# Kernel tuning notes

Hardware: AMD Instinct MI355X
Metric: run time of the kernel (lower is better)

## Reference

```python
import jax, jax.numpy as jnp
import numpy as np

EPS = 1e-17       # utils.EPS in tkipf/compile
NEG_INF = -1e30   # utils.NEG_INF
B, T, V, H, L, S = 256, 128, 512, 256, 64, 4
TEMP_B = 1.0


def setup_inputs() -> dict:
    key = jax.random.key(0)
    ks = jax.random.split(key, 12)

    def lin(k, o, i):  # torch nn.Linear default init: U(-1/sqrt(in), 1/sqrt(in))
        s = 1.0 / np.sqrt(i)
        kw, kb = jax.random.split(k)
        return (jax.random.uniform(kw, (o, i), jnp.float32, -s, s),
                jax.random.uniform(kb, (o,), jnp.float32, -s, s))

    w_ih, b_ih = lin(ks[0], 4 * H, H)   # LSTMCell input weights (i,f,g,o)
    w_hh, b_hh = lin(ks[1], 4 * H, H)
    wz1, bz1 = lin(ks[2], H, H)         # head_z_1
    wz2, bz2 = lin(ks[3], 2 * L, H)     # head_z_2 (gaussian: mu, log_var)
    wb1, bb1 = lin(ks[4], H, H)         # head_b_1
    wb2, bb2 = lin(ks[5], 1, H)         # head_b_2
    wd1, bd1 = lin(ks[6], H, L)         # decode_1
    wd2, bd2 = lin(ks[7], V, H)         # decode_2
    embed_w = jax.random.normal(ks[8], (V, H), jnp.float32)  # nn.Embedding N(0,1)
    inputs = jax.random.randint(ks[9], (B, T), 0, V)
    lengths = jax.random.randint(ks[10], (B,), 1, T + 1)
    return dict(embed_w=embed_w, w_ih=w_ih, w_hh=w_hh, b_ih=b_ih, b_hh=b_hh,
                wz1=wz1, bz1=bz1, wz2=wz2, bz2=bz2, wb1=wb1, bb1=bb1,
                wb2=wb2, bb2=bb2, wd1=wd1, bd1=bd1, wd2=wd2, bd2=bd2,
                inputs=inputs, lengths=lengths)


def _forward(embed_w, w_ih, w_hh, b_ih, b_hh, wz1, bz1, wz2, bz2,
             wb1, bb1, wb2, bb2, wd1, bd1, wd2, bd2, inputs, lengths):
    nkey = jax.random.key(42)  # fixed sampling noise (training path, evaluate=False)
    emb = embed_w[inputs]      # [B,T,H]

    def lstm_step(carry, xm):
        h, c = carry
        x, m = xm              # x: [B,H], m: [B] mask for this step
        gates = x @ w_ih.T + b_ih + h @ w_hh.T + b_hh
        i, f, g, o = jnp.split(gates, 4, axis=1)
        c2 = jax.nn.sigmoid(f) * c + jax.nn.sigmoid(i) * jnp.tanh(g)
        h2 = jax.nn.sigmoid(o) * jnp.tanh(c2)
        h2 = m[:, None] * h2
        c2 = m[:, None] * c2
        return (h2, c2), h2

    def masked_encode(mask):
        init = (jnp.zeros((B, H), emb.dtype), jnp.zeros((B, H), emb.dtype))
        _, hs = jax.lax.scan(lstm_step, init, (emb.transpose(1, 0, 2), mask.T))
        return hs.transpose(1, 0, 2)  # [B,T,H]

    mask = jnp.ones((B, T), jnp.float32)
    log_cum_acc = jnp.zeros((B, T), jnp.float32)  # sum of log-cumsums over segments
    encs, recs, masks = [], [], []
    b_logits, b_samples, z_logits, z_samples = [], [], [], []

    for seg in range(S):  # small fixed structural loop (max_num_segments)
        enc = masked_encode(mask)
        encs.append(enc)

        # --- boundaries b ---
        if seg == S - 1:
            sample_b = jax.nn.one_hot(lengths - 1, T, dtype=jnp.float32)
        else:
            hid = jax.nn.relu(enc @ wb1.T + bb1)
            lb = (hid @ wb2.T + bb2)[..., 0]  # [B,T]
            lb = jnp.concatenate([jnp.full((B, 1), NEG_INF, jnp.float32), lb[:, 1:]], axis=1)
            u = jax.random.uniform(jax.random.fold_in(nkey, 2 * seg), (B, T), jnp.float32)
            gumbel = -jnp.log(EPS - jnp.log(u + EPS))
            sample_b = jax.nn.softmax((lb + gumbel) / TEMP_B, axis=-1)
            b_logits.append(lb)
        b_samples.append(sample_b)

        # --- latents z (gaussian) ---
        readout = jnp.sum(enc[:, :-1] * sample_b[:, 1:, None], axis=1)  # [B,H]
        lz = jax.nn.relu(readout @ wz1.T + bz1) @ wz2.T + bz2           # [B,2L]
        mu, log_var = jnp.split(lz, 2, axis=1)
        eps_z = jax.random.normal(jax.random.fold_in(nkey, 2 * seg + 1), (B, L), jnp.float32)
        sample_z = mu + jnp.exp(0.5 * log_var) * eps_z
        z_logits.append(lz)
        z_samples.append(sample_z)

        # --- next-segment hidden-state mask: prod of cumsums (in log space) ---
        log_cum_acc = log_cum_acc + jnp.log(jnp.cumsum(sample_b, axis=1) + EPS)
        if seg < S - 1:
            mask = jnp.exp(log_cum_acc)
            masks.append(mask)

        # --- decode: single step repeated over full sequence ---
        pred = jax.nn.relu(sample_z @ wd1.T + bd1) @ wd2.T + bd2        # [B,V]
        recs.append(jnp.broadcast_to(pred[:, None, :], (B, T, V)))

    return (jnp.stack(encs), jnp.stack(recs), jnp.stack(masks),
            jnp.stack(b_logits), jnp.stack(b_samples),
            jnp.stack(z_logits), jnp.stack(z_samples))


def reference(embed_w, w_ih, w_hh, b_ih, b_hh, wz1, bz1, wz2, bz2,
              wb1, bb1, wb2, bb2, wd1, bd1, wd2, bd2, inputs, lengths):
    return _forward(embed_w, w_ih, w_hh, b_ih, b_hh, wz1, bz1, wz2, bz2,
                    wb1, bb1, wb2, bb2, wd1, bd1, wd2, bd2, inputs, lengths)
```

## Files before the change

kernel.cpp:

```cpp
#include <hip/hip_runtime.h>
#include <hip/hip_bf16.h>

#define RNG_VARIANT 2

typedef __attribute__((ext_vector_type(8))) short bf16x8;
typedef __attribute__((ext_vector_type(4))) float f32x4;

__host__ __device__ inline void tf2x32(unsigned k0, unsigned k1,
                                       unsigned x0, unsigned x1,
                                       unsigned* r0, unsigned* r1) {
  unsigned ks2 = k0 ^ k1 ^ 0x1BD11BDAu;
#define TFR(r) { x0 += x1; x1 = (x1 << r) | (x1 >> (32 - r)); x1 ^= x0; }
  x0 += k0; x1 += k1;
  TFR(13) TFR(15) TFR(26) TFR(6)  x0 += k1;  x1 += ks2 + 1u;
  TFR(17) TFR(29) TFR(16) TFR(24) x0 += ks2; x1 += k0 + 2u;
  TFR(13) TFR(15) TFR(26) TFR(6)  x0 += k0;  x1 += k1 + 3u;
  TFR(17) TFR(29) TFR(16) TFR(24) x0 += k1;  x1 += ks2 + 4u;
  TFR(13) TFR(15) TFR(26) TFR(6)  x0 += ks2; x1 += k0 + 5u;
#undef TFR
  *r0 = x0; *r1 = x1;
}

__device__ __forceinline__ unsigned rng_bits32(unsigned k0, unsigned k1,
                                               unsigned n, unsigned half) {
#if RNG_VARIANT == 2
  unsigned o0, o1; tf2x32(k0, k1, 0u, n, &o0, &o1); return o0 ^ o1;
#elif RNG_VARIANT == 1
  unsigned o0, o1; tf2x32(k0, k1, 0u, n, &o0, &o1); return o1;
#else
  unsigned i0 = (n < half) ? n : n - half;
  unsigned o0, o1; tf2x32(k0, k1, i0, i0 + half, &o0, &o1);
  return (n < half) ? o0 : o1;
#endif
}

__device__ __forceinline__ float bits_to_unit(unsigned bits) {
  return __uint_as_float((bits >> 9) | 0x3f800000u) - 1.0f;
}

__device__ __forceinline__ unsigned short f2bf(float x) {
  union { float f; unsigned u; } v; v.f = x;
  unsigned r = v.u + 0x7fffu + ((v.u >> 16) & 1u);
  return (unsigned short)(r >> 16);
}
__device__ __forceinline__ float bf2f(unsigned short h) {
  return __uint_as_float(((unsigned)h) << 16);
}

__device__ __forceinline__ float sigm(float x) {
  return 1.0f / (1.0f + __expf(-x));
}
__device__ __forceinline__ float tanh_f(float x) {
  float ax = fabsf(x);
  float e = __expf(-2.0f * ax);
  float t = (1.0f - e) / (1.0f + e);
  return copysignf(t, x);
}

__device__ __forceinline__ float erfinv_f(float x) {
  float w = -log1pf(-x * x);
  float p;
  if (w < 5.0f) {
    w -= 2.5f;
    p = 2.81022636e-08f;
    p = fmaf(p, w, 3.43273939e-07f);
    p = fmaf(p, w, -3.5233877e-06f);
    p = fmaf(p, w, -4.39150654e-06f);
    p = fmaf(p, w, 0.00021858087f);
    p = fmaf(p, w, -0.00125372503f);
    p = fmaf(p, w, -0.00417768164f);
    p = fmaf(p, w, 0.246640727f);
    p = fmaf(p, w, 1.50140941f);
  } else {
    w = sqrtf(w) - 3.0f;
    p = -0.000200214257f;
    p = fmaf(p, w, 0.000100950558f);
    p = fmaf(p, w, 0.00134934322f);
    p = fmaf(p, w, -0.00367342844f);
    p = fmaf(p, w, 0.00573950773f);
    p = fmaf(p, w, -0.0076224613f);
    p = fmaf(p, w, 0.00943887047f);
    p = fmaf(p, w, 1.00167406f);
    p = fmaf(p, w, 2.83297682f);
  }
  return p * x;
}

__global__ void prep_k(const float* __restrict__ w_ih, const float* __restrict__ w_hh,
                       const float* __restrict__ wb1, const float* __restrict__ b_ih,
                       const float* __restrict__ b_hh,
                       unsigned short* __restrict__ wih_b, unsigned short* __restrict__ wpk,
                       unsigned short* __restrict__ wb1_b, float* __restrict__ biasg,
                       unsigned int* __restrict__ flags) {
  int i = blockIdx.x * 256 + threadIdx.x;
  for (int idx = i; idx < 262144; idx += 65536) wih_b[idx] = f2bf(w_ih[idx]);
  if (i < 65536) wb1_b[i] = f2bf(wb1[i]);
  if (i < 1024) biasg[i] = b_ih[i] + b_hh[i];
  if (i >= 1024 && i < 2048) flags[i - 1024] = 0u;
  if (i < 32768) {
    int l = i & 63, ks = (i >> 6) & 7, tile = i >> 9;
    int n = tile * 16 + (l & 15);
    int kb = ks * 32 + (l >> 4) * 8;
    const float* src = w_hh + (size_t)n * 256 + kb;
#pragma unroll
    for (int j = 0; j < 8; ++j) wpk[(size_t)i * 8 + j] = f2bf(src[j]);
  }
}

__global__ void embed_k(const int* __restrict__ inputs, const float* __restrict__ embw,
                        unsigned short* __restrict__ emb) {
  int bt = blockIdx.x, h = threadIdx.x;
  emb[(size_t)bt * 256 + h] = f2bf(embw[(size_t)inputs[bt] * 256 + h]);
}

__global__ __launch_bounds__(256) void gemm_bf16(
    const unsigned short* __restrict__ A, const unsigned short* __restrict__ Bt,
    const float* __restrict__ bias, float* __restrict__ outF,
    unsigned short* __restrict__ outB, int M, int N, int K, int relu) {
  __shared__ __align__(16) unsigned short As[128][40];
  __shared__ __align__(16) unsigned short Bs[128][40];
  int tid = threadIdx.x;
  int m0 = blockIdx.x * 128, n0 = blockIdx.y * 128;
  int w = tid >> 6, l = tid & 63;
  int wr = w >> 1, wc = w & 1;
  int lr = l & 15, lq = l >> 4;
  f32x4 acc[4][4];
#pragma unroll
  for (int i = 0; i < 4; ++i)
#pragma unroll
    for (int j = 0; j < 4; ++j) acc[i][j] = (f32x4)(0.0f);
  int sr = tid >> 2, sk = (tid & 3) * 8;
#pragma unroll 1
  for (int kc = 0; kc < K; kc += 32) {
#pragma unroll
    for (int p = 0; p < 2; ++p) {
      int row = sr + p * 64;
      *(bf16x8*)&As[row][sk] = *(const bf16x8*)(A + (size_t)(m0 + row) * K + kc + sk);
      *(bf16x8*)&Bs[row][sk] = *(const bf16x8*)(Bt + (size_t)(n0 + row) * K + kc + sk);
    }
    __syncthreads();
    bf16x8 af[4], bfr[4];
#pragma unroll
    for (int i = 0; i < 4; ++i) {
      af[i] = *(const bf16x8*)&As[wr * 64 + i * 16 + lr][lq * 8];
      bfr[i] = *(const bf16x8*)&Bs[wc * 64 + i * 16 + lr][lq * 8];
    }
#pragma unroll
    for (int i = 0; i < 4; ++i)
#pragma unroll
      for (int j = 0; j < 4; ++j)
        acc[i][j] = __builtin_amdgcn_mfma_f32_16x16x32_bf16(af[i], bfr[j], acc[i][j], 0, 0, 0);
    __syncthreads();
  }
#pragma unroll
  for (int i = 0; i < 4; ++i)
#pragma unroll
    for (int j = 0; j < 4; ++j) {
      int col = n0 + wc * 64 + j * 16 + lr;
      float bv = bias ? bias[col] : 0.0f;
#pragma unroll
      for (int q = 0; q < 4; ++q) {
        int row = m0 + wr * 64 + i * 16 + lq * 4 + q;
        float v = acc[i][j][q] + bv;
        if (relu) v = fmaxf(v, 0.0f);
        size_t o = (size_t)row * N + col;
        if (outF) outF[o] = v;
        if (outB) outB[o] = f2bf(v);
      }
    }
}

template <bool XWF32>
__global__ __launch_bounds__(256, 1) void lstm_lds(
    const unsigned short* __restrict__ Wpk, const void* __restrict__ xw_,
    const float* __restrict__ mask_buf, int use_mask,
    float* __restrict__ enc_out, unsigned short* __restrict__ enc_b,
    unsigned int* flags, unsigned int flag_base) {
  __shared__ __align__(16) unsigned short Wl[65536];
  const int tid = threadIdx.x;
  const int w = tid >> 6, l = tid & 63;
  const int lr = l & 15, lq = l >> 4;
  const int rg = blockIdx.x >> 2, cb = blockIdx.x & 3;
  const int batch = rg * 16 + lr;
  const int nsub = cb * 64 + w * 16 + lq * 4;

  {
    const int4* src4 = (const int4*)Wpk;
    int4* dst4 = (int4*)Wl;
#pragma unroll
    for (int it = 0; it < 32; ++it) {
      int d = tid + it * 256;
      int tile = d >> 9, within = d & 511;
      int g = tile >> 2, wv = tile & 3;
      dst4[d] = src4[(size_t)(g * 16 + cb * 4 + wv) * 512 + within];
    }
  }
  __syncthreads();

  float cst[4] = {0.f, 0.f, 0.f, 0.f};
  unsigned int* flag = flags + rg * 64;

  const float* xwf = (const float*)xw_;
  const unsigned short* xwb = (const unsigned short*)xw_;
  f32x4 xwf4[4];
  uint2 xwu2[4];
  float mvp;

#define PREFETCH(T)                                                          \
  {                                                                          \
    size_t base_ = ((size_t)batch * 128 + (T)) * 1024 + nsub;                \
    _Pragma("unroll") for (int g = 0; g < 4; ++g) {                          \
      if (XWF32)                                                             \
        xwf4[g] = *(const f32x4*)(xwf + base_ + g * 256);                    \
      else                                                                   \
        xwu2[g] = *(const uint2*)(xwb + base_ + g * 256);                    \
    }                                                                        \
    mvp = use_mask ? mask_buf[batch * 128 + (T)] : 1.0f;                     \
  }

  PREFETCH(0);

#pragma unroll 1
  for (int t = 0; t < 128; ++t) {
    f32x4 acc[4];
#pragma unroll
    for (int g = 0; g < 4; ++g) {
      if (XWF32) {
        acc[g] = xwf4[g];
      } else {
        acc[g][0] = __uint_as_float(xwu2[g].x << 16);
        acc[g][1] = __uint_as_float(xwu2[g].x & 0xffff0000u);
        acc[g][2] = __uint_as_float(xwu2[g].y << 16);
        acc[g][3] = __uint_as_float(xwu2[g].y & 0xffff0000u);
      }
    }
    float mv = mvp;

    if (t < 127) PREFETCH(t + 1);

    int woff = 0;
    asm volatile("" : "+v"(woff));
    bf16x8 Wf[4][8];
#pragma unroll
    for (int g = 0; g < 4; ++g)
#pragma unroll
      for (int ks = 0; ks < 8; ++ks)
        Wf[g][ks] = *(const bf16x8*)(Wl + woff + ((g * 4 + w) << 12) +
                                     (ks << 9) + (l << 3));
#pragma unroll
    for (int g = 0; g < 4; ++g)
#pragma unroll
      for (int ks = 0; ks < 8; ++ks)
        asm volatile("" : "+v"(Wf[g][ks]));

    if (t > 0) {
      unsigned thr = flag_base + 4u * (unsigned)t;
      while (__hip_atomic_load(flag, __ATOMIC_RELAXED, __HIP_MEMORY_SCOPE_AGENT) < thr)
        __builtin_amdgcn_s_sleep(1);
      const unsigned short* hrow = enc_b + ((size_t)batch * 128 + (t - 1)) * 256;
      bf16x8 af[8];
#pragma unroll
      for (int ks = 0; ks < 8; ++ks)
        af[ks] = *(const bf16x8*)(hrow + ks * 32 + lq * 8);
#pragma unroll
      for (int ks = 0; ks < 8; ++ks)
#pragma unroll
        for (int g = 0; g < 4; ++g)
          acc[g] = __builtin_amdgcn_mfma_f32_16x16x32_bf16(Wf[g][ks], af[ks],
                                                           acc[g], 0, 0, 0);
    }

    float hv[4];
#pragma unroll
    for (int q = 0; q < 4; ++q) {
      float ig = acc[0][q], fg = acc[1][q], gg = acc[2][q], og = acc[3][q];
      float cn = sigm(fg) * cst[q] + sigm(ig) * tanh_f(gg);
      float hq = sigm(og) * tanh_f(cn);
      hq *= mv;
      cn *= mv;
      cst[q] = cn;
      hv[q] = hq;
    }
    size_t eo = ((size_t)batch * 128 + t) * 256 + nsub;
    f32x4 hvv;
    hvv[0] = hv[0]; hvv[1] = hv[1]; hvv[2] = hv[2]; hvv[3] = hv[3];
    *(f32x4*)(enc_out + eo) = hvv;
    unsigned long long pk =
        (unsigned long long)f2bf(hv[0]) |
        ((unsigned long long)f2bf(hv[1]) << 16) |
        ((unsigned long long)f2bf(hv[2]) << 32) |
        ((unsigned long long)f2bf(hv[3]) << 48);
    __hip_atomic_store((unsigned long long*)(enc_b + eo), pk,
                       __ATOMIC_RELAXED, __HIP_MEMORY_SCOPE_AGENT);

    asm volatile("s_waitcnt vmcnt(0)" ::: "memory");
    __syncthreads();
    if (tid == 0)
      __hip_atomic_fetch_add(flag, 1u, __ATOMIC_RELAXED, __HIP_MEMORY_SCOPE_AGENT);
  }
#undef PREFETCH
}

__global__ __launch_bounds__(512) void gemv_lb(const unsigned short* __restrict__ hid,
                                               const float* __restrict__ wb2,
                                               const float* __restrict__ bb2,
                                               float* __restrict__ lb) {
  int l = threadIdx.x & 63, w = threadIdx.x >> 6;
  int row = blockIdx.x * 8 + w;
  const unsigned short* hp = hid + (size_t)row * 256 + l * 4;
  uint2 hv = *(const uint2*)hp;
  float4 wv = *(const float4*)(wb2 + l * 4);
  float s = bf2f((unsigned short)(hv.x & 0xffff)) * wv.x +
            bf2f((unsigned short)(hv.x >> 16)) * wv.y +
            bf2f((unsigned short)(hv.y & 0xffff)) * wv.z +
            bf2f((unsigned short)(hv.y >> 16)) * wv.w;
#pragma unroll
  for (int d = 32; d > 0; d >>= 1) s += __shfl_xor(s, d);
  if (l == 0) lb[row] = s + bb2[0];
}

__global__ __launch_bounds__(128) void boundary_k(
    const float* __restrict__ lb, int seg, unsigned k0, unsigned k1,
    float* __restrict__ blog, float* __restrict__ bsamp, float* __restrict__ masks_o,
    float* __restrict__ lca, float* __restrict__ maskb) {
  int b = blockIdx.x, t = threadIdx.x;
  int l = t & 63, w = t >> 6;
  float v = lb[b * 128 + t];
  if (t == 0) v = -1e30f;
  unsigned bits = rng_bits32(k0, k1, (unsigned)(b * 128 + t), 16384u);
  float u = bits_to_unit(bits);
  float g = -logf(1e-17f - logf(u + 1e-17f));
  float y = v + g;
  float m = y;
#pragma unroll
  for (int d = 32; d > 0; d >>= 1) m = fmaxf(m, __shfl_xor(m, d));
  __shared__ float xs[2];
  if (l == 0) xs[w] = m;
  __syncthreads();
  m = fmaxf(xs[0], xs[1]);
  float e = expf(y - m);
  float ssum = e;
#pragma unroll
  for (int d = 32; d > 0; d >>= 1) ssum += __shfl_xor(ssum, d);
  __shared__ float ss2[2];
  if (l == 0) ss2[w] = ssum;
  __syncthreads();
  ssum = ss2[0] + ss2[1];
  float sb = e / ssum;
  blog[b * 128 + t] = v;
  bsamp[b * 128 + t] = sb;
  float cs = sb;
#pragma unroll
  for (int d = 1; d < 64; d <<= 1) {
    float p = __shfl_up(cs, d);
    if (l >= d) cs += p;
  }
  __shared__ float wt[2];
  if (l == 63) wt[w] = cs;
  __syncthreads();
  if (w == 1) cs += wt[0];
  float lg = logf(cs + 1e-17f);
  float a = (seg == 0 ? 0.0f : lca[b * 128 + t]) + lg;
  lca[b * 128 + t] = a;
  float mk = expf(a);
  maskb[b * 128 + t] = mk;
  masks_o[b * 128 + t] = mk;
}

__global__ __launch_bounds__(128) void onehot_k(const int* __restrict__ lengths,
                                                float* __restrict__ bsamp) {
  int b = blockIdx.x, t = threadIdx.x;
  bsamp[b * 128 + t] = (t == lengths[b] - 1) ? 1.0f : 0.0f;
}

__global__ __launch_bounds__(256) void readout_k(const float* __restrict__ enc,
                                                 const float* __restrict__ sb,
                                                 float* __restrict__ rout) {
  int b = blockIdx.x, h = threadIdx.x;
  __shared__ float sl[128];
  if (h < 128) sl[h] = sb[b * 128 + h];
  __syncthreads();
  float a = 0.0f;
  const float* ep = enc + (size_t)b * 128 * 256 + h;
#pragma unroll 4
  for (int t2 = 0; t2 < 127; ++t2) a += ep[(size_t)t2 * 256] * sl[t2 + 1];
  rout[b * 256 + h] = a;
}

__global__ __launch_bounds__(128) void zhead_k(
    const float* __restrict__ rout, const float* __restrict__ wz1,
    const float* __restrict__ bz1, const float* __restrict__ wz2,
    const float* __restrict__ bz2, unsigned k0, unsigned k1,
    float* __restrict__ zlo, float* __restrict__ zsa, float* __restrict__ zbuf) {
  int b = blockIdx.x, t = threadIdx.x;
  __shared__ float rl[256], hz[256], lzs[128];
  rl[t] = rout[b * 256 + t];
  rl[t + 128] = rout[b * 256 + t + 128];
  __syncthreads();
  for (int h = t; h < 256; h += 128) {
    float a = bz1[h];
    const float* wp = wz1 + (size_t)h * 256;
    for (int k2 = 0; k2 < 256; ++k2) a += rl[k2] * wp[k2];
    hz[h] = fmaxf(a, 0.0f);
  }
  __syncthreads();
  {
    float a = bz2[t];
    const float* wp = wz2 + (size_t)t * 256;
    for (int k2 = 0; k2 < 256; ++k2) a += hz[k2] * wp[k2];
    zlo[b * 128 + t] = a;
    lzs[t] = a;
  }
  __syncthreads();
  if (t < 64) {
    unsigned bits = rng_bits32(k0, k1, (unsigned)(b * 64 + t), 8192u);
    float f = bits_to_unit(bits);
    const float LO = -0x1.fffffep-1f;
    float u = fmaxf(LO, f * 2.0f + LO);
    float ez = 1.4142135623730951f * erfinv_f(u);
    float z = lzs[t] + expf(0.5f * lzs[t + 64]) * ez;
    zsa[b * 64 + t] = z;
    zbuf[b * 64 + t] = z;
  }
}

__global__ __launch_bounds__(256) void decode_k(
    const float* __restrict__ zbuf, const float* __restrict__ wd1,
    const float* __restrict__ bd1, const float* __restrict__ wd2,
    const float* __restrict__ bd2, float* __restrict__ pred) {
  int b = blockIdx.x, t = threadIdx.x;
  __shared__ float zl[64], hd[256];
  if (t < 64) zl[t] = zbuf[b * 64 + t];
  __syncthreads();
  {
    float a = bd1[t];
    const float* wp = wd1 + (size_t)t * 64;
    for (int k2 = 0; k2 < 64; ++k2) a += zl[k2] * wp[k2];
    hd[t] = fmaxf(a, 0.0f);
  }
  __syncthreads();
  for (int v2 = t; v2 < 512; v2 += 256) {
    float p = bd2[v2];
    const float* wp = wd2 + (size_t)v2 * 256;
    for (int k2 = 0; k2 < 256; ++k2) p += hd[k2] * wp[k2];
    pred[b * 512 + v2] = p;
  }
}

__global__ __launch_bounds__(128) void bcast_k(const float* __restrict__ pred,
                                               float* __restrict__ recs) {
  int bt = blockIdx.x;
  int b = bt >> 7;
  float4 v = ((const float4*)(pred + (size_t)b * 512))[threadIdx.x];
  ((float4*)(recs + (size_t)bt * 512))[threadIdx.x] = v;
}

extern "C" void kernel_launch(void* const* d_in, const int* in_sizes, int n_in,
                              void* d_out, int out_size, void* d_ws, size_t ws_size,
                              hipStream_t stream) {
  const float* embed_w = (const float*)d_in[0];
  const float* w_ih = (const float*)d_in[1];
  const float* w_hh = (const float*)d_in[2];
  const float* b_ih = (const float*)d_in[3];
  const float* b_hh = (const float*)d_in[4];
  const float* wz1 = (const float*)d_in[5];
  const float* bz1 = (const float*)d_in[6];
  const float* wz2 = (const float*)d_in[7];
  const float* bz2 = (const float*)d_in[8];
  const float* wb1 = (const float*)d_in[9];
  const float* bb1 = (const float*)d_in[10];
  const float* wb2 = (const float*)d_in[11];
  const float* bb2 = (const float*)d_in[12];
  const float* wd1 = (const float*)d_in[13];
  const float* bd1 = (const float*)d_in[14];
  const float* wd2 = (const float*)d_in[15];
  const float* bd2 = (const float*)d_in[16];
  const int* inputs = (const int*)d_in[17];
  const int* lengths = (const int*)d_in[18];

  char* ws = (char*)d_ws;
  size_t off = 0;
  auto alloc = [&](size_t n) { char* p = ws + off; off += (n + 255) & ~(size_t)255; return p; };
  unsigned short* wih_b = (unsigned short*)alloc((size_t)1024 * 256 * 2);
  unsigned short* wpk   = (unsigned short*)alloc((size_t)1024 * 256 * 2);
  unsigned short* wb1_b = (unsigned short*)alloc((size_t)256 * 256 * 2);
  float* biasg = (float*)alloc(1024 * 4);
  unsigned int* flags = (unsigned int*)alloc(1024 * 4);
  unsigned short* bufA  = (unsigned short*)alloc((size_t)32768 * 256 * 2);
  unsigned short* enc_b = (unsigned short*)alloc((size_t)32768 * 256 * 2);
  float* lb    = (float*)alloc((size_t)32768 * 4);
  float* lca   = (float*)alloc((size_t)32768 * 4);
  float* maskb = (float*)alloc((size_t)32768 * 4);
  float* rout  = (float*)alloc((size_t)256 * 256 * 4);
  float* zbuf  = (float*)alloc((size_t)256 * 64 * 4);
  float* pred  = (float*)alloc((size_t)256 * 512 * 4);
  size_t fixed = off;
  bool xwf32 = (ws_size >= fixed + (size_t)32768 * 1024 * 4);
  void* xw = alloc(xwf32 ? (size_t)32768 * 1024 * 4 : (size_t)32768 * 1024 * 2);

  unsigned kb[4][2], kz[4][2];
  for (int s = 0; s < 4; ++s) {
    tf2x32(0u, 42u, 0u, (unsigned)(2 * s), &kb[s][0], &kb[s][1]);
    tf2x32(0u, 42u, 0u, (unsigned)(2 * s + 1), &kz[s][0], &kz[s][1]);
  }

  float* out = (float*)d_out;
  float* encs = out;
  float* recs = out + 33554432;
  float* masks = out + 100663296;
  float* blog = out + 100761600;
  float* bsamp = out + 100859904;
  float* zlog = out + 100990976;
  float* zsamp = out + 101122048;

  prep_k<<<256, 256, 0, stream>>>(w_ih, w_hh, wb1, b_ih, b_hh, wih_b, wpk, wb1_b,
                                  biasg, flags);
  embed_k<<<32768, 256, 0, stream>>>(inputs, embed_w, bufA);
  {
    dim3 g(32768 / 128, 1024 / 128);
    gemm_bf16<<<g, 256, 0, stream>>>(bufA, wih_b, biasg,
                                     xwf32 ? (float*)xw : nullptr,
                                     xwf32 ? nullptr : (unsigned short*)xw,
                                     32768, 1024, 256, 0);
  }

  for (int seg = 0; seg < 4; ++seg) {
    unsigned fb = (unsigned)seg * 512u;
    if (xwf32)
      lstm_lds<true><<<64, 256, 0, stream>>>(wpk, xw, maskb, seg > 0 ? 1 : 0,
                                             encs + (size_t)seg * 8388608, enc_b,
                                             flags, fb);
    else
      lstm_lds<false><<<64, 256, 0, stream>>>(wpk, xw, maskb, seg > 0 ? 1 : 0,
                                              encs + (size_t)seg * 8388608, enc_b,
                                              flags, fb);

    if (seg < 3) {
      dim3 g(32768 / 128, 256 / 128);
      gemm_bf16<<<g, 256, 0, stream>>>(enc_b, wb1_b, bb1, nullptr, bufA,
                                       32768, 256, 256, 1);
      gemv_lb<<<4096, 512, 0, stream>>>(bufA, wb2, bb2, lb);
      boundary_k<<<256, 128, 0, stream>>>(lb, seg, kb[seg][0], kb[seg][1],
                                          blog + (size_t)seg * 32768,
                                          bsamp + (size_t)seg * 32768,
                                          masks + (size_t)seg * 32768, lca, maskb);
    } else {
      onehot_k<<<256, 128, 0, stream>>>(lengths, bsamp + (size_t)3 * 32768);
    }
    readout_k<<<256, 256, 0, stream>>>(encs + (size_t)seg * 8388608,
                                       bsamp + (size_t)seg * 32768, rout);
    zhead_k<<<256, 128, 0, stream>>>(rout, wz1, bz1, wz2, bz2, kz[seg][0], kz[seg][1],
                                     zlog + (size_t)seg * 32768,
                                     zsamp + (size_t)seg * 16384, zbuf);
    decode_k<<<256, 256, 0, stream>>>(zbuf, wd1, bd1, wd2, bd2, pred);
    bcast_k<<<32768, 128, 0, stream>>>(pred, recs + (size_t)seg * 16777216);
  }
}
```

Measured before the change: 2.105 ms.

## Replace per-step counter flags with sentinel-value polling on LSTM hidden state

The per-step atomic counter handshake between the blocks of a row group is removed. Each consumer now polls the previous step's hidden-state values directly, treating a 0xffff bf16 pattern as 'not yet written'. Before every segment a fill kernel resets enc_b to that sentinel, and the block-to-(row,col) mapping is changed. This drops the waitcnt, block barrier and atomic increment from each of the 128 serial steps, at the cost of an extra 16MB fill per segment and a correctness risk if a real hidden value ever encodes as 0xffff.

```diff
diff --git a/kernel.cpp b/kernel.cpp
--- a/kernel.cpp
+++ b/kernel.cpp
@@ -90,13 +90,11 @@
                        const float* __restrict__ wb1, const float* __restrict__ b_ih,
                        const float* __restrict__ b_hh,
                        unsigned short* __restrict__ wih_b, unsigned short* __restrict__ wpk,
-                       unsigned short* __restrict__ wb1_b, float* __restrict__ biasg,
-                       unsigned int* __restrict__ flags) {
+                       unsigned short* __restrict__ wb1_b, float* __restrict__ biasg) {
   int i = blockIdx.x * 256 + threadIdx.x;
   for (int idx = i; idx < 262144; idx += 65536) wih_b[idx] = f2bf(w_ih[idx]);
   if (i < 65536) wb1_b[i] = f2bf(wb1[i]);
   if (i < 1024) biasg[i] = b_ih[i] + b_hh[i];
-  if (i >= 1024 && i < 2048) flags[i - 1024] = 0u;
   if (i < 32768) {
     int l = i & 63, ks = (i >> 6) & 7, tile = i >> 9;
     int n = tile * 16 + (l & 15);
@@ -111,6 +109,11 @@
                         unsigned short* __restrict__ emb) {
   int bt = blockIdx.x, h = threadIdx.x;
   emb[(size_t)bt * 256 + h] = f2bf(embw[(size_t)inputs[bt] * 256 + h]);
+}
+
+__global__ void fill_sent(uint4* __restrict__ p) {
+  uint4 v; v.x = v.y = v.z = v.w = 0xffffffffu;
+  p[blockIdx.x * 256 + threadIdx.x] = v;
 }
 
 __global__ __launch_bounds__(256) void gemm_bf16(
@@ -171,16 +174,15 @@
 }
 
 template <bool XWF32>
-__global__ __launch_bounds__(256, 1) void lstm_lds(
+__global__ __launch_bounds__(256, 1) void lstm_poll(
     const unsigned short* __restrict__ Wpk, const void* __restrict__ xw_,
     const float* __restrict__ mask_buf, int use_mask,
-    float* __restrict__ enc_out, unsigned short* __restrict__ enc_b,
-    unsigned int* flags, unsigned int flag_base) {
+    float* __restrict__ enc_out, unsigned short* __restrict__ enc_b) {
   __shared__ __align__(16) unsigned short Wl[65536];
   const int tid = threadIdx.x;
   const int w = tid >> 6, l = tid & 63;
   const int lr = l & 15, lq = l >> 4;
-  const int rg = blockIdx.x >> 2, cb = blockIdx.x & 3;
+  const int rg = blockIdx.x & 15, cb = blockIdx.x >> 4;
   const int batch = rg * 16 + lr;
   const int nsub = cb * 64 + w * 16 + lq * 4;
 
@@ -198,7 +200,6 @@
   __syncthreads();
 
   float cst[4] = {0.f, 0.f, 0.f, 0.f};
-  unsigned int* flag = flags + rg * 64;
 
   const float* xwf = (const float*)xw_;
   const unsigned short* xwb = (const unsigned short*)xw_;
@@ -254,14 +255,31 @@
         asm volatile("" : "+v"(Wf[g][ks]));
 
     if (t > 0) {
-      unsigned thr = flag_base + 4u * (unsigned)t;
-      while (__hip_atomic_load(flag, __ATOMIC_RELAXED, __HIP_MEMORY_SCOPE_AGENT) < thr)
-        __builtin_amdgcn_s_sleep(1);
-      const unsigned short* hrow = enc_b + ((size_t)batch * 128 + (t - 1)) * 256;
+      const unsigned long long* hq =
+          (const unsigned long long*)(enc_b + ((size_t)batch * 128 + (t - 1)) * 256);
+      unsigned long long rv[16];
+      while (true) {
+#pragma unroll
+        for (int i = 0; i < 8; ++i) {
+          rv[2 * i] = __hip_atomic_load(hq + i * 8 + lq * 2,
+                                        __ATOMIC_RELAXED, __HIP_MEMORY_SCOPE_AGENT);
+          rv[2 * i + 1] = __hip_atomic_load(hq + i * 8 + lq * 2 + 1,
+                                            __ATOMIC_RELAXED, __HIP_MEMORY_SCOPE_AGENT);
+        }
+        unsigned bad = 0;
+#pragma unroll
+        for (int i = 0; i < 16; ++i)
+          bad |= (((unsigned)rv[i] & 0xffffu) == 0xffffu) ? 1u : 0u;
+        if (!__any(bad)) break;
+      }
       bf16x8 af[8];
 #pragma unroll
-      for (int ks = 0; ks < 8; ++ks)
-        af[ks] = *(const bf16x8*)(hrow + ks * 32 + lq * 8);
+      for (int i = 0; i < 8; ++i) {
+        union { unsigned long long u[2]; bf16x8 v; } cv;
+        cv.u[0] = rv[2 * i];
+        cv.u[1] = rv[2 * i + 1];
+        af[i] = cv.v;
+      }
 #pragma unroll
       for (int ks = 0; ks < 8; ++ks)
 #pragma unroll
@@ -275,11 +293,11 @@
     for (int q = 0; q < 4; ++q) {
       float ig = acc[0][q], fg = acc[1][q], gg = acc[2][q], og = acc[3][q];
       float cn = sigm(fg) * cst[q] + sigm(ig) * tanh_f(gg);
-      float hq = sigm(og) * tanh_f(cn);
-      hq *= mv;
+      float hq2 = sigm(og) * tanh_f(cn);
+      hq2 *= mv;
       cn *= mv;
       cst[q] = cn;
-      hv[q] = hq;
+      hv[q] = hq2;
     }
     size_t eo = ((size_t)batch * 128 + t) * 256 + nsub;
     f32x4 hvv;
@@ -292,11 +310,6 @@
         ((unsigned long long)f2bf(hv[3]) << 48);
     __hip_atomic_store((unsigned long long*)(enc_b + eo), pk,
                        __ATOMIC_RELAXED, __HIP_MEMORY_SCOPE_AGENT);
-
-    asm volatile("s_waitcnt vmcnt(0)" ::: "memory");
-    __syncthreads();
-    if (tid == 0)
-      __hip_atomic_fetch_add(flag, 1u, __ATOMIC_RELAXED, __HIP_MEMORY_SCOPE_AGENT);
   }
 #undef PREFETCH
 }
@@ -485,7 +498,6 @@
   unsigned short* wpk   = (unsigned short*)alloc((size_t)1024 * 256 * 2);
   unsigned short* wb1_b = (unsigned short*)alloc((size_t)256 * 256 * 2);
   float* biasg = (float*)alloc(1024 * 4);
-  unsigned int* flags = (unsigned int*)alloc(1024 * 4);
   unsigned short* bufA  = (unsigned short*)alloc((size_t)32768 * 256 * 2);
   unsigned short* enc_b = (unsigned short*)alloc((size_t)32768 * 256 * 2);
   float* lb    = (float*)alloc((size_t)32768 * 4);
@@ -513,8 +525,7 @@
   float* zlog = out + 100990976;
   float* zsamp = out + 101122048;
 
-  prep_k<<<256, 256, 0, stream>>>(w_ih, w_hh, wb1, b_ih, b_hh, wih_b, wpk, wb1_b,
-                                  biasg, flags);
+  prep_k<<<256, 256, 0, stream>>>(w_ih, w_hh, wb1, b_ih, b_hh, wih_b, wpk, wb1_b, biasg);
   embed_k<<<32768, 256, 0, stream>>>(inputs, embed_w, bufA);
   {
     dim3 g(32768 / 128, 1024 / 128);
@@ -525,15 +536,13 @@
   }
 
   for (int seg = 0; seg < 4; ++seg) {
-    unsigned fb = (unsigned)seg * 512u;
+    fill_sent<<<4096, 256, 0, stream>>>((uint4*)enc_b);
     if (xwf32)
-      lstm_lds<true><<<64, 256, 0, stream>>>(wpk, xw, maskb, seg > 0 ? 1 : 0,
-                                             encs + (size_t)seg * 8388608, enc_b,
-                                             flags, fb);
+      lstm_poll<true><<<64, 256, 0, stream>>>(wpk, xw, maskb, seg > 0 ? 1 : 0,
+                                              encs + (size_t)seg * 8388608, enc_b);
     else
-      lstm_lds<false><<<64, 256, 0, stream>>>(wpk, xw, maskb, seg > 0 ? 1 : 0,
-                                              encs + (size_t)seg * 8388608, enc_b,
-                                              flags, fb);
+      lstm_poll<false><<<64, 256, 0, stream>>>(wpk, xw, maskb, seg > 0 ? 1 : 0,
+                                               encs + (size_t)seg * 8388608, enc_b);
 
     if (seg < 3) {
       dim3 g(32768 / 128, 256 / 128);
```

Measured after the change: 3.078 ms. +46.2%, slower.

## Replace block barrier with per-wave flag increments and hoist LDS weight loads

Applied to the files above, without the earlier changes.

Each wave now bumps the cross-block row-group flag on its own, so the block-wide __syncthreads before the flag increment goes away. The threshold becomes 16 per step and the per-segment flag base grows to match. The spin loop drops its s_sleep, the LDS weight fragment loads and the h loads are hoisted ahead of the xw prefetch with scheduling barriers, and the fp32 encoder store moves after the bf16 handoff store. The block-to-row-group mapping is also changed so the four column blocks of a row group are spread across the grid. The busy spin without sleep may add memory contention, and it relies on per-wave vmcnt waits for ordering.

```diff
diff --git a/kernel.cpp b/kernel.cpp
--- a/kernel.cpp
+++ b/kernel.cpp
@@ -171,7 +171,7 @@
 }
 
 template <bool XWF32>
-__global__ __launch_bounds__(256, 1) void lstm_lds(
+__global__ __launch_bounds__(256, 1) void lstm_flag(
     const unsigned short* __restrict__ Wpk, const void* __restrict__ xw_,
     const float* __restrict__ mask_buf, int use_mask,
     float* __restrict__ enc_out, unsigned short* __restrict__ enc_b,
@@ -180,7 +180,7 @@
   const int tid = threadIdx.x;
   const int w = tid >> 6, l = tid & 63;
   const int lr = l & 15, lq = l >> 4;
-  const int rg = blockIdx.x >> 2, cb = blockIdx.x & 3;
+  const int rg = blockIdx.x & 15, cb = blockIdx.x >> 4;
   const int batch = rg * 16 + lr;
   const int nsub = cb * 64 + w * 16 + lq * 4;
 
@@ -222,6 +222,36 @@
 
 #pragma unroll 1
   for (int t = 0; t < 128; ++t) {
+    int woff = 0;
+    asm volatile("" : "+v"(woff));
+    bf16x8 Wf[4][8];
+#pragma unroll
+    for (int g = 0; g < 4; ++g)
+#pragma unroll
+      for (int ks = 0; ks < 8; ++ks)
+        Wf[g][ks] = *(const bf16x8*)(Wl + woff + ((g * 4 + w) << 12) +
+                                     (ks << 9) + (l << 3));
+#pragma unroll
+    for (int g = 0; g < 4; ++g)
+#pragma unroll
+      for (int ks = 0; ks < 8; ++ks)
+        asm volatile("" : "+v"(Wf[g][ks]));
+
+    bf16x8 af[8];
+    if (t > 0) {
+      unsigned thr = flag_base + 16u * (unsigned)t;
+      unsigned fv;
+      while ((fv = __hip_atomic_load(flag, __ATOMIC_RELAXED,
+                                     __HIP_MEMORY_SCOPE_AGENT)) < thr) { }
+      asm volatile("" : "+v"(fv));
+      const unsigned short* hrow =
+          enc_b + ((size_t)batch * 128 + (t - 1)) * 256 + (fv >> 31);
+#pragma unroll
+      for (int ks = 0; ks < 8; ++ks)
+        af[ks] = *(const bf16x8*)(hrow + ks * 32 + lq * 8);
+    }
+    __builtin_amdgcn_sched_barrier(0);
+
     f32x4 acc[4];
 #pragma unroll
     for (int g = 0; g < 4; ++g) {
@@ -235,33 +265,10 @@
       }
     }
     float mv = mvp;
-
     if (t < 127) PREFETCH(t + 1);
-
-    int woff = 0;
-    asm volatile("" : "+v"(woff));
-    bf16x8 Wf[4][8];
-#pragma unroll
-    for (int g = 0; g < 4; ++g)
-#pragma unroll
-      for (int ks = 0; ks < 8; ++ks)
-        Wf[g][ks] = *(const bf16x8*)(Wl + woff + ((g * 4 + w) << 12) +
-                                     (ks << 9) + (l << 3));
-#pragma unroll
-    for (int g = 0; g < 4; ++g)
-#pragma unroll
-      for (int ks = 0; ks < 8; ++ks)
-        asm volatile("" : "+v"(Wf[g][ks]));
+    __builtin_amdgcn_sched_barrier(0);
 
     if (t > 0) {
-      unsigned thr = flag_base + 4u * (unsigned)t;
-      while (__hip_atomic_load(flag, __ATOMIC_RELAXED, __HIP_MEMORY_SCOPE_AGENT) < thr)
-        __builtin_amdgcn_s_sleep(1);
-      const unsigned short* hrow = enc_b + ((size_t)batch * 128 + (t - 1)) * 256;
-      bf16x8 af[8];
-#pragma unroll
-      for (int ks = 0; ks < 8; ++ks)
-        af[ks] = *(const bf16x8*)(hrow + ks * 32 + lq * 8);
 #pragma unroll
       for (int ks = 0; ks < 8; ++ks)
 #pragma unroll
@@ -275,16 +282,13 @@
     for (int q = 0; q < 4; ++q) {
       float ig = acc[0][q], fg = acc[1][q], gg = acc[2][q], og = acc[3][q];
       float cn = sigm(fg) * cst[q] + sigm(ig) * tanh_f(gg);
-      float hq = sigm(og) * tanh_f(cn);
-      hq *= mv;
+      float hq2 = sigm(og) * tanh_f(cn);
+      hq2 *= mv;
       cn *= mv;
       cst[q] = cn;
-      hv[q] = hq;
+      hv[q] = hq2;
     }
     size_t eo = ((size_t)batch * 128 + t) * 256 + nsub;
-    f32x4 hvv;
-    hvv[0] = hv[0]; hvv[1] = hv[1]; hvv[2] = hv[2]; hvv[3] = hv[3];
-    *(f32x4*)(enc_out + eo) = hvv;
     unsigned long long pk =
         (unsigned long long)f2bf(hv[0]) |
         ((unsigned long long)f2bf(hv[1]) << 16) |
@@ -292,11 +296,14 @@
         ((unsigned long long)f2bf(hv[3]) << 48);
     __hip_atomic_store((unsigned long long*)(enc_b + eo), pk,
                        __ATOMIC_RELAXED, __HIP_MEMORY_SCOPE_AGENT);
+    f32x4 hvv;
+    hvv[0] = hv[0]; hvv[1] = hv[1]; hvv[2] = hv[2]; hvv[3] = hv[3];
+    *(f32x4*)(enc_out + eo) = hvv;
 
     asm volatile("s_waitcnt vmcnt(0)" ::: "memory");
-    __syncthreads();
-    if (tid == 0)
+    if (l == 0)
       __hip_atomic_fetch_add(flag, 1u, __ATOMIC_RELAXED, __HIP_MEMORY_SCOPE_AGENT);
+    __builtin_amdgcn_sched_barrier(0);
   }
 #undef PREFETCH
 }
@@ -525,15 +532,15 @@
   }
 
   for (int seg = 0; seg < 4; ++seg) {
-    unsigned fb = (unsigned)seg * 512u;
+    unsigned fb = (unsigned)seg * 2048u;
     if (xwf32)
-      lstm_lds<true><<<64, 256, 0, stream>>>(wpk, xw, maskb, seg > 0 ? 1 : 0,
-                                             encs + (size_t)seg * 8388608, enc_b,
-                                             flags, fb);
-    else
-      lstm_lds<false><<<64, 256, 0, stream>>>(wpk, xw, maskb, seg > 0 ? 1 : 0,
+      lstm_flag<true><<<64, 256, 0, stream>>>(wpk, xw, maskb, seg > 0 ? 1 : 0,
                                               encs + (size_t)seg * 8388608, enc_b,
                                               flags, fb);
+    else
+      lstm_flag<false><<<64, 256, 0, stream>>>(wpk, xw, maskb, seg > 0 ? 1 : 0,
+                                               encs + (size_t)seg * 8388608, enc_b,
+                                               flags, fb);
 
     if (seg < 3) {
       dim3 g(32768 / 128, 256 / 128);
```

New measurement: 2.167 ms. 1.03x slower.
